# Kernel tuning notes

Hardware: AMD Instinct MI355X
Metric: run time of the kernel (lower is better)

## Reference

```python
import jax, jax.numpy as jnp
import numpy as np

NUM_HEADS = 16
ROPE_BASE = 10000.0
NEG_INF = float('-inf')


def _rotate_half_interleaved(x):
    # x: [..., d]; interleaved rotation: (-x2, x1) pairs
    x1 = x[..., ::2]
    x2 = x[..., 1::2]
    return jnp.stack((-x2, x1), axis=-1).reshape(x.shape)


def _rope_tables(seq_len, head_dim, dtype):
    inv_freq = 1.0 / (ROPE_BASE ** (jnp.arange(0, head_dim, 2, dtype=jnp.float32) / head_dim))
    pos = jnp.arange(seq_len, dtype=jnp.float32)
    freqs = pos[:, None] * inv_freq[None, :]          # [S, d/2]
    emb = jnp.concatenate((freqs, freqs), axis=-1)    # [S, d]  (HF-style concat, as in source)
    return jnp.cos(emb).astype(dtype), jnp.sin(emb).astype(dtype)


def setup_inputs() -> dict:
    key = jax.random.key(0)
    ks = jax.random.split(key, 4)
    B, S, H = 2, 2048, 2048
    scale = 0.02
    x = jax.random.normal(ks[0], (B, S, H), dtype=jnp.float32)
    qkv_w = jax.random.normal(ks[1], (3 * H, H), dtype=jnp.float32) * scale
    qkv_b = jnp.zeros((3 * H,), dtype=jnp.float32)
    out_w = jax.random.normal(ks[2], (H, H), dtype=jnp.float32) * scale
    out_b = jnp.zeros((H,), dtype=jnp.float32)
    attention_mask = jnp.ones((B, S), dtype=jnp.int32)
    return {"x": x, "attention_mask": attention_mask, "qkv_w": qkv_w,
            "qkv_b": qkv_b, "out_w": out_w, "out_b": out_b}


def reference(x, attention_mask, qkv_w, qkv_b, out_w, out_b):
    B, S, H = x.shape
    nh = NUM_HEADS
    hd = H // nh
    scale = hd ** -0.5

    qkv = x @ qkv_w.T + qkv_b                            # [B,S,3H]
    qkv = qkv.reshape(B, S, 3, nh, hd).transpose(2, 0, 3, 1, 4)  # [3,B,nh,S,hd]
    q, k, v = qkv[0], qkv[1], qkv[2]

    cos, sin = _rope_tables(S, hd, x.dtype)              # [S,hd]
    cos = cos[None, None, :, :]
    sin = sin[None, None, :, :]
    q = q * cos + _rotate_half_interleaved(q) * sin
    k = k * cos + _rotate_half_interleaved(k) * sin

    scores = jnp.einsum('bhqd,bhkd->bhqk', q, k) * scale  # [B,nh,S,S]
    causal = jnp.triu(jnp.ones((S, S), dtype=bool), k=1)
    scores = jnp.where(causal[None, None], NEG_INF, scores)
    key_mask = (attention_mask == 0)[:, None, None, :]    # [B,1,1,S]
    scores = jnp.where(key_mask, NEG_INF, scores)

    weights = jax.nn.softmax(scores, axis=-1)
    attn = jnp.einsum('bhqk,bhkd->bhqd', weights, v)       # [B,nh,S,hd]
    attn = attn.transpose(0, 2, 1, 3).reshape(B, S, H)
    return attn @ out_w.T + out_b
```

## Files before the change

### kernel.cpp

```cpp
#include <hip/hip_runtime.h>

typedef __bf16 bf16;
typedef __bf16 bf16x2 __attribute__((ext_vector_type(2)));
typedef __bf16 bf16x4 __attribute__((ext_vector_type(4)));
typedef __bf16 bf16x8 __attribute__((ext_vector_type(8)));
typedef float f32x4 __attribute__((ext_vector_type(4)));
typedef float f32x16 __attribute__((ext_vector_type(16)));

#define MFMA_BF16(a, b, c) __builtin_amdgcn_mfma_f32_16x16x32_bf16(a, b, c, 0, 0, 0)
#define MFMA32(a, b, c)    __builtin_amdgcn_mfma_f32_32x32x16_bf16(a, b, c, 0, 0, 0)

__device__ __forceinline__ void async16(const void* g, void* l) {
    __builtin_amdgcn_global_load_lds(
        (const __attribute__((address_space(1))) void*)g,
        (__attribute__((address_space(3))) void*)l,
        16, 0, 0);
}

__device__ __forceinline__ unsigned pack2(float a, float b) {
    bf16x2 t; t[0] = (bf16)a; t[1] = (bf16)b;
    return __builtin_bit_cast(unsigned, t);
}

__device__ __forceinline__ void cvt8_body(const float* __restrict__ in,
                                          bf16* __restrict__ out, int blk) {
    int i = (blk * 256 + (int)threadIdx.x) * 8;
    float4 a = *(const float4*)(in + i);
    float4 b = *(const float4*)(in + i + 4);
    bf16x8 o;
    o[0] = (bf16)a.x; o[1] = (bf16)a.y; o[2] = (bf16)a.z; o[3] = (bf16)a.w;
    o[4] = (bf16)b.x; o[5] = (bf16)b.y; o[6] = (bf16)b.z; o[7] = (bf16)b.w;
    *(bf16x8*)(out + i) = o;
}

__global__ void prep(const float* __restrict__ x, const float* __restrict__ qkvw,
                     const float* __restrict__ outw, const int* __restrict__ am,
                     bf16* __restrict__ xb, bf16* __restrict__ wqkv, bf16* __restrict__ wout,
                     float* __restrict__ cosT, float* __restrict__ sinT,
                     float* __restrict__ mbias) {
    int blk = blockIdx.x;
    if (blk < 4096)        cvt8_body(x,    xb,   blk);
    else if (blk < 10240)  cvt8_body(qkvw, wqkv, blk - 4096);
    else if (blk < 12288)  cvt8_body(outw, wout, blk - 10240);
    else {
        int i = (blk - 12288) * 256 + threadIdx.x;
        int s = i >> 7, d = i & 127, fi = d & 63;
        float inv = exp2f(-(float)fi * (13.287712379549449f / 64.0f));
        float ang = (float)s * inv;
        cosT[i] = cosf(ang);
        sinT[i] = sinf(ang);
        if (i < 2 * 2048) mbias[i] = (am[i] == 0) ? -1.4427e30f : 0.0f;
    }
}

template <int EPI>
__global__ void __launch_bounds__(256, 2)
gemm_bt(const bf16* __restrict__ A, const bf16* __restrict__ Bt,
        const float* __restrict__ bias, float* __restrict__ Cf,
        bf16* __restrict__ qb, bf16* __restrict__ kb, bf16* __restrict__ vtb,
        const float* __restrict__ cosT, const float* __restrict__ sinT,
        int M, int N, int K) {
    __shared__ __align__(16) bf16 sA[128 * 64];
    __shared__ __align__(16) bf16 sB[128 * 64];
    const int tid  = threadIdx.x;
    const int lane = tid & 63;
    const int quad = lane >> 4, l15 = lane & 15;
    const int wid = tid >> 6, wm = wid >> 1, wn = wid & 1;
    const int bm = blockIdx.x, bn = blockIdx.y;

    f32x4 acc[4][4];
#pragma unroll
    for (int i = 0; i < 4; i++)
#pragma unroll
        for (int j = 0; j < 4; j++)
#pragma unroll
            for (int c = 0; c < 4; c++) acc[i][j][c] = 0.0f;

    const int r0 = tid >> 3, x0 = tid & 7;
    const int g0 = x0 ^ (r0 & 7);
    const bf16* pa = A  + (size_t)(bm * 128 + r0) * K + g0 * 8;
    const bf16* pb = Bt + (size_t)(bn * 128 + r0) * K + g0 * 8;
    bf16* la = sA + tid * 8;
    bf16* lb = sB + tid * 8;
    const size_t gstep = (size_t)32 * K;

    for (int k0 = 0; k0 < K; k0 += 64) {
#pragma unroll
        for (int i = 0; i < 4; i++) {
            async16(pa + i * gstep, la + i * 2048);
            async16(pb + i * gstep, lb + i * 2048);
        }
        pa += 64; pb += 64;
        __syncthreads();
#pragma unroll
        for (int ks = 0; ks < 2; ks++) {
            bf16x8 af[4], bfr[4];
#pragma unroll
            for (int i = 0; i < 4; i++) {
                int r = wm * 64 + i * 16 + l15;
                int x = (ks * 4 + quad) ^ (r & 7);
                af[i] = *(const bf16x8*)(sA + r * 64 + x * 8);
            }
#pragma unroll
            for (int i = 0; i < 4; i++) {
                int r = wn * 64 + i * 16 + l15;
                int x = (ks * 4 + quad) ^ (r & 7);
                bfr[i] = *(const bf16x8*)(sB + r * 64 + x * 8);
            }
#pragma unroll
            for (int mi = 0; mi < 4; mi++)
#pragma unroll
                for (int ni = 0; ni < 4; ni++)
                    acc[mi][ni] = MFMA_BF16(af[mi], bfr[ni], acc[mi][ni]);
        }
        __syncthreads();
    }

    if (EPI == 0) {
#pragma unroll
        for (int mi = 0; mi < 4; mi++)
#pragma unroll
            for (int ni = 0; ni < 4; ni++) {
                int row0 = bm * 128 + wm * 64 + mi * 16 + quad * 4;
                int col  = bn * 128 + wn * 64 + ni * 16 + l15;
                float bv = bias[col];
#pragma unroll
                for (int r = 0; r < 4; r++)
                    Cf[(size_t)(row0 + r) * N + col] = acc[mi][ni][r] + bv;
            }
    } else {
#pragma unroll
        for (int mi = 0; mi < 4; mi++)
#pragma unroll
            for (int ni = 0; ni < 4; ni++) {
                int col   = bn * 128 + wn * 64 + ni * 16 + l15;
                int which = col >> 11;
                int hcol  = col & 2047;
                int h = hcol >> 7, d = hcol & 127;
                float bv = bias[col];
#pragma unroll
                for (int r = 0; r < 4; r++) {
                    int row = bm * 128 + wm * 64 + mi * 16 + quad * 4 + r;
                    int b = row >> 11, s = row & 2047;
                    float v  = acc[mi][ni][r] + bv;
                    float vp = __shfl_xor(v, 1, 64);
                    float ov = v;
                    if (which < 2) {
                        float c  = cosT[(s << 7) + d];
                        float sn = sinT[(s << 7) + d];
                        ov = v * c + ((d & 1) ? vp : -vp) * sn;
                    }
                    if (which == 0) ov *= 0.12751743f;
                    size_t bh = (size_t)(b * 16 + h);
                    if (which == 0)      qb[(bh * 2048 + s) * 128 + d] = (bf16)ov;
                    else if (which == 1) kb[(bh * 2048 + s) * 128 + d] = (bf16)ov;
                    else                 vtb[(bh * 128 + d) * 2048 + s] = (bf16)ov;
                }
            }
    }
}

__global__ void __launch_bounds__(256, 2)
fattn(const bf16* __restrict__ Q, const bf16* __restrict__ Kg,
      const bf16* __restrict__ Vt, const float* __restrict__ mbias,
      bf16* __restrict__ O, float* __restrict__ Opart, float* __restrict__ mlpart) {
    __shared__ __align__(16) bf16 sK[2][64 * 128];
    __shared__ __align__(16) bf16 sV[2][128 * 64];
    __shared__ __align__(16) float sMB[2048];
    const int tid = threadIdx.x, lane = tid & 63, w = tid >> 6;
    const int l31 = lane & 31, half = lane >> 5;
    const int id = (int)blockIdx.x;
    const int bh = id & 31, v = id >> 5;
    const int p = v >> 1, role = v & 1;
    const int qa = 15 - p;
    const int n1 = role ? (15 - 2 * p) : 17;

    const bf16* Qb  = Q  + (size_t)bh * 2048 * 128;
    const bf16* Kbh = Kg + (size_t)bh * 2048 * 128;
    const bf16* Vbh = Vt + (size_t)bh * 128 * 2048;
    const int b = bh >> 4, hh = bh & 15;
    const float* mbb = mbias + b * 2048;

    const int swk = (l31 & 15) ^ (l31 >> 4);
    const int swv = (l31 & 7) ^ ((l31 >> 3) & 3);
    const int rk = tid >> 4, xk = tid & 15, gkb = xk ^ rk;
    const int rv = tid >> 3, xv = tid & 7;
    const int gv = xv ^ (rv & 7) ^ ((rv >> 3) & 3);

    auto KT = [&](int t) { return role ? (t < n1 ? 17 + t : t - n1) : t; };

    int qt = qa;
    int myq  = qt * 128 + w * 32 + l31;
    int qmin = qt * 128 + w * 32;

    bf16x8 qf[8];
#pragma unroll
    for (int kq = 0; kq < 8; kq++)
        qf[kq] = *(const bf16x8*)(Qb + (size_t)myq * 128 + kq * 16 + half * 8);

    f32x16 oacc[4];
#pragma unroll
    for (int dt = 0; dt < 4; dt++)
#pragma unroll
        for (int c = 0; c < 16; c++) oacc[dt][c] = 0.0f;
    float m_s = -3e38f, l_s = 0.0f;

    {
        float4 t0 = *(const float4*)(mbb + tid * 8);
        float4 t1 = *(const float4*)(mbb + tid * 8 + 4);
        *(float4*)(sMB + tid * 8) = t0;
        *(float4*)(sMB + tid * 8 + 4) = t1;
    }

    {
        int kb0 = KT(0) * 64;
#pragma unroll
        for (int i = 0; i < 4; i++) {
            async16(Kbh + (size_t)(kb0 + rk + i * 16) * 128 + (gkb ^ (i & 1)) * 8,
                    &sK[0][(i * 256 + tid) * 8]);
            async16(Vbh + (size_t)(rv + i * 32) * 2048 + kb0 + gv * 8,
                    &sV[0][(i * 256 + tid) * 8]);
        }
    }
    __syncthreads();

    for (int t = 0; t < 17; t++) {
        if (role && t == n1) {
            float lf = l_s + __shfl_xor(l_s, 32, 64);
            size_t slot = (size_t)(bh * 8 + (qa - 8)) * 2 + 1;
            float* op = Opart + slot * 16384 + (size_t)(w * 32 + l31) * 128;
#pragma unroll
            for (int dt = 0; dt < 4; dt++)
#pragma unroll
                for (int g = 0; g < 4; g++) {
                    float4 o4 = make_float4(oacc[dt][g * 4 + 0], oacc[dt][g * 4 + 1],
                                            oacc[dt][g * 4 + 2], oacc[dt][g * 4 + 3]);
                    *(float4*)(op + dt * 32 + 8 * g + 4 * half) = o4;
                }
            if (half == 0) {
                float* mp = mlpart + (slot * 128 + (w * 32 + l31)) * 2;
                mp[0] = m_s; mp[1] = lf;
            }
#pragma unroll
            for (int dt = 0; dt < 4; dt++)
#pragma unroll
                for (int c = 0; c < 16; c++) oacc[dt][c] = 0.0f;
            m_s = -3e38f; l_s = 0.0f;
            qt = p;
            myq  = qt * 128 + w * 32 + l31;
            qmin = qt * 128 + w * 32;
#pragma unroll
            for (int kq = 0; kq < 8; kq++)
                qf[kq] = *(const bf16x8*)(Qb + (size_t)myq * 128 + kq * 16 + half * 8);
        }

        const int kb0 = KT(t) * 64;
        const int buf = t & 1;
        if (t + 1 < 17) {
            const int nb0 = KT(t + 1) * 64;
#pragma unroll
            for (int i = 0; i < 4; i++) {
                async16(Kbh + (size_t)(nb0 + rk + i * 16) * 128 + (gkb ^ (i & 1)) * 8,
                        &sK[buf ^ 1][(i * 256 + tid) * 8]);
                async16(Vbh + (size_t)(rv + i * 32) * 2048 + nb0 + gv * 8,
                        &sV[buf ^ 1][(i * 256 + tid) * 8]);
            }
        }
        const bf16* sKb = sK[buf];
        const bf16* sVb = sV[buf];

        f32x16 sacc[2];
#pragma unroll
        for (int tt = 0; tt < 2; tt++)
#pragma unroll
            for (int c = 0; c < 16; c++) sacc[tt][c] = 0.0f;
        __builtin_amdgcn_s_setprio(1);
#pragma unroll
        for (int kq = 0; kq < 8; kq++) {
#pragma unroll
            for (int tt = 0; tt < 2; tt++) {
                int row = tt * 32 + l31;
                int x = (kq * 2 + half) ^ swk;
                bf16x8 kf = *(const bf16x8*)(sKb + row * 128 + x * 8);
                sacc[tt] = MFMA32(kf, qf[kq], sacc[tt]);
            }
        }
        __builtin_amdgcn_s_setprio(0);

        float mx = -3e38f;
        if (kb0 + 63 < qmin) {
#pragma unroll
            for (int tt = 0; tt < 2; tt++)
#pragma unroll
                for (int g = 0; g < 4; g++) {
                    float4 mb4 = *(const float4*)(sMB + kb0 + tt * 32 + 8 * g + 4 * half);
#pragma unroll
                    for (int r2 = 0; r2 < 4; r2++) {
                        float vv = sacc[tt][g * 4 + r2] + ((const float*)&mb4)[r2];
                        sacc[tt][g * 4 + r2] = vv;
                        mx = fmaxf(mx, vv);
                    }
                }
        } else {
#pragma unroll
            for (int tt = 0; tt < 2; tt++)
#pragma unroll
                for (int g = 0; g < 4; g++) {
                    float4 mb4 = *(const float4*)(sMB + kb0 + tt * 32 + 8 * g + 4 * half);
#pragma unroll
                    for (int r2 = 0; r2 < 4; r2++) {
                        int sk = kb0 + tt * 32 + 8 * g + 4 * half + r2;
                        float vv = sacc[tt][g * 4 + r2] + ((const float*)&mb4)[r2];
                        vv = (sk > myq) ? -1e30f : vv;
                        sacc[tt][g * 4 + r2] = vv;
                        mx = fmaxf(mx, vv);
                    }
                }
        }

        mx = fmaxf(mx, __shfl_xor(mx, 32, 64));
        float mnew = fmaxf(m_s, mx);
        if (__all(mx - m_s <= 8.0f)) mnew = m_s;
        float alpha = exp2f(m_s - mnew);
        float rs = 0.0f;
#pragma unroll
        for (int tt = 0; tt < 2; tt++)
#pragma unroll
            for (int c = 0; c < 16; c++) {
                float pe = exp2f(sacc[tt][c] - mnew);
                sacc[tt][c] = pe;
                rs += pe;
            }
        l_s = l_s * alpha + rs;
        if (mnew > m_s) {
#pragma unroll
            for (int dt = 0; dt < 4; dt++) oacc[dt] *= alpha;
        }
        m_s = mnew;

#pragma unroll
        for (int tt = 0; tt < 2; tt++) {
            unsigned w8[8];
#pragma unroll
            for (int i = 0; i < 8; i++)
                w8[i] = pack2(sacc[tt][2 * i], sacc[tt][2 * i + 1]);
#pragma unroll
            for (int s2 = 0; s2 < 2; s2++) {
                const int bse = 4 * s2;
                unsigned a0 = half ? w8[bse]     : w8[bse + 2];
                unsigned a1 = half ? w8[bse + 1] : w8[bse + 3];
                unsigned z0 = (unsigned)__shfl_xor((int)a0, 32, 64);
                unsigned z1 = (unsigned)__shfl_xor((int)a1, 32, 64);
                union { unsigned u[4]; bf16x8 vv; } pu;
                pu.u[0] = half ? z0 : w8[bse];
                pu.u[1] = half ? z1 : w8[bse + 1];
                pu.u[2] = half ? w8[bse + 2] : z0;
                pu.u[3] = half ? w8[bse + 3] : z1;
                bf16x8 pf = pu.vv;
                const int c = (tt * 2 + s2) * 2 + half;
                __builtin_amdgcn_s_setprio(1);
#pragma unroll
                for (int dt = 0; dt < 4; dt++) {
                    int row = dt * 32 + l31;
                    int x = c ^ swv;
                    bf16x8 vf = *(const bf16x8*)(sVb + row * 64 + x * 8);
                    oacc[dt] = MFMA32(vf, pf, oacc[dt]);
                }
                __builtin_amdgcn_s_setprio(0);
            }
        }
        __syncthreads();
    }

    float lf = l_s + __shfl_xor(l_s, 32, 64);
    if (role == 0) {
        size_t slot = (size_t)(bh * 8 + (qa - 8)) * 2 + 0;
        float* op = Opart + slot * 16384 + (size_t)(w * 32 + l31) * 128;
#pragma unroll
        for (int dt = 0; dt < 4; dt++)
#pragma unroll
            for (int g = 0; g < 4; g++) {
                float4 o4 = make_float4(oacc[dt][g * 4 + 0], oacc[dt][g * 4 + 1],
                                        oacc[dt][g * 4 + 2], oacc[dt][g * 4 + 3]);
                *(float4*)(op + dt * 32 + 8 * g + 4 * half) = o4;
            }
        if (half == 0) {
            float* mp = mlpart + (slot * 128 + (w * 32 + l31)) * 2;
            mp[0] = m_s; mp[1] = lf;
        }
    } else {
        float inv = 1.0f / lf;
        size_t base = ((size_t)(b * 2048 + myq)) * 2048 + hh * 128;
#pragma unroll
        for (int dt = 0; dt < 4; dt++)
#pragma unroll
            for (int g = 0; g < 4; g++) {
                bf16x4 o4;
#pragma unroll
                for (int r2 = 0; r2 < 4; r2++) o4[r2] = (bf16)(oacc[dt][g * 4 + r2] * inv);
                *(bf16x4*)(O + base + dt * 32 + 8 * g + 4 * half) = o4;
            }
    }
}

__global__ void combine(const float* __restrict__ Opart, const float* __restrict__ mlpart,
                        bf16* __restrict__ attn) {
    int i = blockIdx.x * 256 + threadIdx.x;
    int dq = (i & 31) * 4;
    int row = i >> 5;
    int qloc = row & 127, ba = row >> 7;
    int ai = ba & 7, bh = ba >> 3;
    const float* mlA = mlpart + ((size_t)(ba * 2 + 0) * 128 + qloc) * 2;
    const float* mlB = mlpart + ((size_t)(ba * 2 + 1) * 128 + qloc) * 2;
    float mA = mlA[0], lA = mlA[1], mB = mlB[0], lB = mlB[1];
    float m = fmaxf(mA, mB);
    float wA = exp2f(mA - m), wB = exp2f(mB - m);
    float inv = 1.0f / (wA * lA + wB * lB);
    float4 oA = *(const float4*)(Opart + (size_t)(ba * 2 + 0) * 16384 + qloc * 128 + dq);
    float4 oB = *(const float4*)(Opart + (size_t)(ba * 2 + 1) * 16384 + qloc * 128 + dq);
    int q = (8 + ai) * 128 + qloc;
    int b = bh >> 4, hh = bh & 15;
    bf16x4 o4;
    o4[0] = (bf16)((wA * oA.x + wB * oB.x) * inv);
    o4[1] = (bf16)((wA * oA.y + wB * oB.y) * inv);
    o4[2] = (bf16)((wA * oA.z + wB * oB.z) * inv);
    o4[3] = (bf16)((wA * oA.w + wB * oB.w) * inv);
    *(bf16x4*)(attn + ((size_t)(b * 2048 + q)) * 2048 + hh * 128 + dq) = o4;
}

extern "C" void kernel_launch(void* const* d_in, const int* in_sizes, int n_in,
                              void* d_out, int out_size, void* d_ws, size_t ws_size,
                              hipStream_t stream) {
    const float* x     = (const float*)d_in[0];
    const int*   am    = (const int*)d_in[1];
    const float* qkvw  = (const float*)d_in[2];
    const float* qkvb  = (const float*)d_in[3];
    const float* outw  = (const float*)d_in[4];
    const float* outb  = (const float*)d_in[5];
    float* out = (float*)d_out;

    char* ws = (char*)d_ws;
    bf16*  xb    = (bf16*)(ws);
    bf16*  wqkv  = (bf16*)(ws + (16ull << 20));
    bf16*  wout  = (bf16*)(ws + (40ull << 20));
    bf16*  qb    = (bf16*)(ws + (48ull << 20));
    bf16*  kb    = (bf16*)(ws + (64ull << 20));
    bf16*  vtb   = (bf16*)(ws + (80ull << 20));
    bf16*  attn  = (bf16*)(ws + (96ull << 20));
    float* cosT  = (float*)(ws + (112ull << 20));
    float* sinT  = (float*)(ws + (113ull << 20));
    float* mbias = (float*)(ws + (114ull << 20));
    float* Opart  = (float*)(ws);
    float* mlpart = (float*)(ws + (32ull << 20));

    prep<<<13312, 256, 0, stream>>>(x, qkvw, outw, am, xb, wqkv, wout, cosT, sinT, mbias);

    gemm_bt<1><<<dim3(32, 48), 256, 0, stream>>>(
        xb, wqkv, qkvb, nullptr, qb, kb, vtb, cosT, sinT, 4096, 6144, 2048);

    fattn<<<dim3(512), 256, 0, stream>>>(qb, kb, vtb, mbias, attn, Opart, mlpart);

    combine<<<4096, 256, 0, stream>>>(Opart, mlpart, attn);

    gemm_bt<0><<<dim3(32, 16), 256, 0, stream>>>(
        attn, wout, outb, out, nullptr, nullptr, nullptr, nullptr, nullptr,
        4096, 2048, 2048);
}
```

Baseline: 385.9 us.

## Add 256x256-tile triple-buffered QKV GEMM kernel with fused RoPE epilogue

Replaces the generic 128x128 gemm_bt QKV projection with a dedicated kernel that uses 256x256 output tiles, 512 threads, and a three-stage async global-to-LDS pipeline with K-step 32. The larger tile raises arithmetic intensity per loaded byte, and the triple buffering overlaps loads with MFMA work. The RoPE, scale and Q/K/V-transpose epilogue is kept. In exchange, the grid shrinks to 384 blocks, so fewer blocks are available to fill the CUs, and register pressure per thread rises.

Measured after the change: 463.6 us. 20.1% more time.

```diff
diff --git a/kernel.cpp b/kernel.cpp
--- a/kernel.cpp
+++ b/kernel.cpp
@@ -51,6 +51,119 @@
         sinT[i] = sinf(ang);
         if (i < 2 * 2048) mbias[i] = (am[i] == 0) ? -1.4427e30f : 0.0f;
     }
+}
+
+__global__ void __launch_bounds__(512, 2)
+qkv256(const bf16* __restrict__ A, const bf16* __restrict__ Bt,
+       const float* __restrict__ bias,
+       bf16* __restrict__ qb, bf16* __restrict__ kb, bf16* __restrict__ vtb,
+       const float* __restrict__ cosT, const float* __restrict__ sinT) {
+    constexpr int K = 2048, NT = K >> 5;
+    __shared__ __align__(16) bf16 sA[3][8192];
+    __shared__ __align__(16) bf16 sB[3][8192];
+    const int tid  = threadIdx.x;
+    const int lane = tid & 63;
+    const int quad = lane >> 4, l15 = lane & 15;
+    const int wid  = tid >> 6, wm = wid >> 2, wn = wid & 3;
+    const int bm = blockIdx.x, bn = blockIdx.y;
+
+    f32x4 acc[8][4];
+#pragma unroll
+    for (int i = 0; i < 8; i++)
+#pragma unroll
+        for (int j = 0; j < 4; j++)
+#pragma unroll
+            for (int c = 0; c < 4; c++) acc[i][j][c] = 0.0f;
+
+    const int trow = tid >> 3;
+    const int u    = (tid & 7) ^ (trow & 7);
+    const int hi   = u >> 2, kc = u & 3;
+    const bf16* pA0 = A  + (size_t)(bm * 256 +      trow + 128 * hi) * K + kc * 8;
+    const bf16* pA1 = A  + (size_t)(bm * 256 + 64 + trow + 128 * hi) * K + kc * 8;
+    const bf16* pB0 = Bt + (size_t)(bn * 256 +      trow + 128 * hi) * K + kc * 8;
+    const bf16* pB1 = Bt + (size_t)(bn * 256 + 64 + trow + 128 * hi) * K + kc * 8;
+    const int ld0 = tid * 8, ld1 = 4096 + tid * 8;
+
+    bf16 *cA = sA[0], *nA = sA[1], *fA = sA[2];
+    bf16 *cB = sB[0], *nB = sB[1], *fB = sB[2];
+
+#define STAGE(DA, DB) do {                                   \
+        async16(pA0, (DA) + ld0); async16(pA1, (DA) + ld1);  \
+        async16(pB0, (DB) + ld0); async16(pB1, (DB) + ld1);  \
+        pA0 += 32; pA1 += 32; pB0 += 32; pB1 += 32;          \
+    } while (0)
+
+    const int xa = ((quad + 4 * wm) ^ (l15 & 7)) * 8;
+    const int xb = ((quad + 4 * (wn >> 1)) ^ (l15 & 7)) * 8;
+    const int ra = l15;
+    const int rb = (wn & 1) * 64 + l15;
+
+    STAGE(cA, cB);
+    STAGE(nA, nB);
+    asm volatile("s_waitcnt vmcnt(4)" ::: "memory");
+    __builtin_amdgcn_sched_barrier(0);
+    __builtin_amdgcn_s_barrier();
+    __builtin_amdgcn_sched_barrier(0);
+
+#pragma unroll 1
+    for (int t = 0; t < NT; ++t) {
+        if (t + 2 < NT) STAGE(fA, fB);
+        {
+            bf16x8 af[8], bv[4];
+#pragma unroll
+            for (int mi = 0; mi < 8; mi++)
+                af[mi] = *(const bf16x8*)(cA + (mi * 16 + ra) * 64 + xa);
+#pragma unroll
+            for (int ni = 0; ni < 4; ni++)
+                bv[ni] = *(const bf16x8*)(cB + (ni * 16 + rb) * 64 + xb);
+#pragma unroll
+            for (int mi = 0; mi < 8; mi++)
+#pragma unroll
+                for (int ni = 0; ni < 4; ni++)
+                    acc[mi][ni] = MFMA_BF16(af[mi], bv[ni], acc[mi][ni]);
+        }
+        __builtin_amdgcn_sched_barrier(0);
+        if (t + 1 < NT) {
+            if (t + 2 < NT) asm volatile("s_waitcnt vmcnt(4)" ::: "memory");
+            else            asm volatile("s_waitcnt vmcnt(0)" ::: "memory");
+            __builtin_amdgcn_sched_barrier(0);
+            __builtin_amdgcn_s_barrier();
+            __builtin_amdgcn_sched_barrier(0);
+        }
+        bf16* tp;
+        tp = cA; cA = nA; nA = fA; fA = tp;
+        tp = cB; cB = nB; nB = fB; fB = tp;
+    }
+#undef STAGE
+
+#pragma unroll
+    for (int mi = 0; mi < 8; mi++)
+#pragma unroll
+        for (int ni = 0; ni < 4; ni++) {
+            int col   = bn * 256 + wn * 64 + ni * 16 + l15;
+            int which = col >> 11;
+            int hcol  = col & 2047;
+            int h = hcol >> 7, d = hcol & 127;
+            float bv = bias[col];
+#pragma unroll
+            for (int r = 0; r < 4; r++) {
+                int row = bm * 256 + wm * 128 + mi * 16 + quad * 4 + r;
+                int b = row >> 11, s = row & 2047;
+                float v  = acc[mi][ni][r] + bv;
+                float vp = __shfl_xor(v, 1, 64);
+                float ov = v;
+                if (which < 2) {
+                    float c  = cosT[(s << 7) + d];
+                    float sn = sinT[(s << 7) + d];
+                    ov = v * c + ((d & 1) ? vp : -vp) * sn;
+                }
+                if (which == 0) ov *= 0.12751743f;
+                size_t bh = (size_t)(b * 16 + h);
+                if (which == 0)      qb[(bh * 2048 + s) * 128 + d] = (bf16)ov;
+                else if (which == 1) kb[(bh * 2048 + s) * 128 + d] = (bf16)ov;
+                else                 vtb[(bh * 128 + d) * 2048 + s] = (bf16)ov;
+            }
+        }
 }
 
 template <int EPI>
@@ -455,8 +568,8 @@
 
     prep<<<13312, 256, 0, stream>>>(x, qkvw, outw, am, xb, wqkv, wout, cosT, sinT, mbias);
 
-    gemm_bt<1><<<dim3(32, 48), 256, 0, stream>>>(
-        xb, wqkv, qkvb, nullptr, qb, kb, vtb, cosT, sinT, 4096, 6144, 2048);
+    qkv256<<<dim3(16, 24), 512, 0, stream>>>(
+        xb, wqkv, qkvb, qb, kb, vtb, cosT, sinT);
 
     fattn<<<dim3(512), 256, 0, stream>>>(qb, kb, vtb, mbias, attn, Opart, mlpart);
 
```
